# Kernel optimization log

Hardware: AMD Instinct MI355X
Metric: run time of the kernel (lower is better)

The kernel has to match this reference:

```python
import jax, jax.numpy as jnp
import numpy as np

NUM_FEAT = 64        # per-head dim == input channel C
HIDDEN = 1024        # total hidden size
NUM_HEADS = HIDDEN // NUM_FEAT  # 16


def setup_inputs() -> dict:
    key = jax.random.key(0)
    k1, k2, k3, k4, k5 = jax.random.split(key, 5)
    B, N, C = 4, 2048, NUM_FEAT
    hidden_states = jax.random.normal(k1, (B, N, C), dtype=jnp.float32)
    # nn.Linear(num_feat, hidden*3): weight [3*hidden, num_feat], store transposed for x @ W
    s_qkv = 1.0 / np.sqrt(C)
    qkv_w = jax.random.uniform(k2, (C, 3 * HIDDEN), jnp.float32, -s_qkv, s_qkv)
    qkv_b = jax.random.uniform(k3, (3 * HIDDEN,), jnp.float32, -s_qkv, s_qkv)
    s_out = 1.0 / np.sqrt(HIDDEN)
    out_w = jax.random.uniform(k4, (HIDDEN, C), jnp.float32, -s_out, s_out)
    out_b = jax.random.uniform(k5, (C,), jnp.float32, -s_out, s_out)
    return {"hidden_states": hidden_states, "qkv_w": qkv_w, "qkv_b": qkv_b,
            "out_w": out_w, "out_b": out_b}


def reference(hidden_states, qkv_w, qkv_b, out_w, out_b):
    B, N, C = hidden_states.shape
    H, D = NUM_HEADS, NUM_FEAT  # head count, head dim
    # qkv projection: [B,N,3*HIDDEN] -> [3,B,H,N,D]
    qkv = hidden_states @ qkv_w + qkv_b
    qkv = qkv.reshape(B, N, 3, H, D).transpose(2, 0, 3, 1, 4)
    q, k, v = qkv[0], qkv[1], qkv[2]
    # scaled dot-product attention with materialized scores (faithful to source)
    scores = jnp.einsum('bhqd,bhkd->bhqk', q, k) / jnp.sqrt(jnp.float32(D))
    probs = jax.nn.softmax(scores, axis=-1)
    ctx = jnp.einsum('bhqk,bhkd->bhqd', probs, v)           # [B,H,N,D]
    ctx = ctx.transpose(0, 2, 1, 3).reshape(B, N, H * D)    # [B,N,HIDDEN]
    out = ctx @ out_w + out_b                               # [B,N,C]
    return jax.nn.gelu(out, approximate=False)
```

## Files before the change

kernel.cpp:

```cpp
#include <hip/hip_runtime.h>
#include <math.h>

#define B_ 4
#define N_ 2048
#define C_ 64
#define H_ 16
#define D_ 64
#define HID 1024

#define QSCALE 0.18033688011112042f

typedef short bf16x8 __attribute__((ext_vector_type(8)));
typedef unsigned short u16x8 __attribute__((ext_vector_type(8)));
typedef float f32x4 __attribute__((ext_vector_type(4)));

#define MFMA(a, b, c) __builtin_amdgcn_mfma_f32_16x16x32_bf16((a), (b), (c), 0, 0, 0)

typedef __attribute__((address_space(3))) void lds_t;
typedef const __attribute__((address_space(1))) void gbl_t;
#define ASYNC16(g, l) __builtin_amdgcn_global_load_lds((gbl_t*)(g), (lds_t*)(l), 16, 0, 0)

static __device__ __forceinline__ unsigned short f2bf(float f) {
  unsigned u = __float_as_uint(f);
  u += 0x7FFFu + ((u >> 16) & 1u);
  return (unsigned short)(u >> 16);
}
static __device__ __forceinline__ float bf2f(unsigned short h) {
  return __uint_as_float((unsigned)h << 16);
}
static __device__ __forceinline__ unsigned pkbf(float a, float b) {
  return __builtin_amdgcn_perm(__float_as_uint(b), __float_as_uint(a),
                               0x07060302u);
}

__global__ __launch_bounds__(256, 2) void qkv_kernel(
    const float* __restrict__ X, const float* __restrict__ W,
    const float* __restrict__ bias, const float* __restrict__ W2,
    unsigned short* __restrict__ Qhi, unsigned short* __restrict__ Khi,
    unsigned short* __restrict__ Vhi,
    unsigned short* __restrict__ W2THi, unsigned short* __restrict__ W2TLo) {
  const int t = threadIdx.x;
  const int ct = blockIdx.x;
  const int tt = blockIdx.y;

  if (ct == 24) {
    int idx0 = tt * 1024 + t * 4;
#pragma unroll
    for (int e = 0; e < 4; ++e) {
      int idx = idx0 + e;
      int k = idx & 1023, col = idx >> 10;
      float v = W2[(size_t)k * 64 + col];
      unsigned short hi = f2bf(v);
      W2THi[(size_t)col * 1024 + k] = hi;
      W2TLo[(size_t)col * 1024 + k] = f2bf(v - bf2f(hi));
    }
    return;
  }

  __shared__ unsigned short qsmem[32768];
  unsigned short* sXhi = qsmem;
  unsigned short* sXlo = qsmem + 8192;
  unsigned short* sWhi = qsmem + 16384;
  unsigned short* sWlo = qsmem + 24576;

  {
    const int kg = t & 7, r0 = t >> 3;
#pragma unroll
    for (int i = 0; i < 4; ++i) {
      int row = r0 + i * 32;
      const float* src = &X[(size_t)(tt * 128 + row) * 64 + kg * 8];
      f32x4 a = *(const f32x4*)src;
      f32x4 b = *(const f32x4*)(src + 4);
      u16x8 hi8, lo8;
#pragma unroll
      for (int j = 0; j < 4; ++j) {
        hi8[j] = f2bf(a[j]);
        lo8[j] = f2bf(a[j] - bf2f(hi8[j]));
        hi8[4 + j] = f2bf(b[j]);
        lo8[4 + j] = f2bf(b[j] - bf2f(hi8[4 + j]));
      }
      int off = row * 64 + ((kg ^ (row & 7)) << 3);
      *(u16x8*)&sXhi[off] = hi8;
      *(u16x8*)&sXlo[off] = lo8;
    }
  }
  {
    const int col = t & 127, kg0 = t >> 7;
#pragma unroll
    for (int i = 0; i < 4; ++i) {
      int kg = kg0 + i * 2;
      u16x8 hi8, lo8;
#pragma unroll
      for (int j = 0; j < 8; ++j) {
        float v = W[(size_t)(kg * 8 + j) * 3072 + ct * 128 + col];
        unsigned short h = f2bf(v);
        hi8[j] = h;
        lo8[j] = f2bf(v - bf2f(h));
      }
      int off = col * 64 + ((kg ^ (col & 7)) << 3);
      *(u16x8*)&sWhi[off] = hi8;
      *(u16x8*)&sWlo[off] = lo8;
    }
  }
  __syncthreads();

  const int w = t >> 6, lane = t & 63;
  const int lid = lane & 15, quad = lane >> 4;

  bf16x8 xa[2][2][2];
#pragma unroll
  for (int mt = 0; mt < 2; ++mt) {
    int row = w * 32 + mt * 16 + lid;
#pragma unroll
    for (int kc = 0; kc < 2; ++kc) {
      int off = row * 64 + (((kc * 4 + quad) ^ (row & 7)) << 3);
      xa[mt][kc][0] = *(const bf16x8*)&sXhi[off];
      xa[mt][kc][1] = *(const bf16x8*)&sXlo[off];
    }
  }

  f32x4 acc[2][8];
#pragma unroll
  for (int mt = 0; mt < 2; ++mt)
#pragma unroll
    for (int nt = 0; nt < 8; ++nt) acc[mt][nt] = (f32x4){0.f, 0.f, 0.f, 0.f};

#pragma unroll
  for (int nt = 0; nt < 8; ++nt) {
    int col = nt * 16 + lid;
#pragma unroll
    for (int kc = 0; kc < 2; ++kc) {
      int boff = col * 64 + (((kc * 4 + quad) ^ (col & 7)) << 3);
      bf16x8 wbh = *(const bf16x8*)&sWhi[boff];
      bf16x8 wbl = *(const bf16x8*)&sWlo[boff];
#pragma unroll
      for (int mt = 0; mt < 2; ++mt) {
        f32x4 c = acc[mt][nt];
        c = MFMA(xa[mt][kc][0], wbh, c);
        c = MFMA(xa[mt][kc][0], wbl, c);
        c = MFMA(xa[mt][kc][1], wbh, c);
        acc[mt][nt] = c;
      }
    }
  }

  __syncthreads();

  const int s = ct >> 3;
  const float scale = (s == 0) ? QSCALE : 1.0f;
  float bias_r[8];
#pragma unroll
  for (int nt = 0; nt < 8; ++nt) bias_r[nt] = bias[ct * 128 + nt * 16 + lid];

  if (s < 2) {
    unsigned short(*sOut)[136] = (unsigned short(*)[136])qsmem;
#pragma unroll
    for (int mt = 0; mt < 2; ++mt)
#pragma unroll
      for (int nt = 0; nt < 8; ++nt) {
        f32x4 v = acc[mt][nt];
#pragma unroll
        for (int r = 0; r < 4; ++r)
          sOut[w * 32 + mt * 16 + quad * 4 + r][nt * 16 + lid] =
              f2bf((v[r] + bias_r[nt]) * scale);
      }
    __syncthreads();
    const int ltok = t >> 1, half = t & 1;
    const int token = tt * 128 + ltok;
    const int bb = token >> 11, n = token & 2047;
    const int head = (ct * 2 + half) & 15;
    unsigned short* A = (s == 0) ? Qhi : Khi;
    size_t dst = ((size_t)(bb * H_ + head) * N_ + n) * D_;
    const unsigned short* srcr = &sOut[ltok][half * 64];
#pragma unroll
    for (int j = 0; j < 8; ++j)
      *(uint4*)&A[dst + j * 8] = *(const uint4*)&srcr[j * 8];
  } else {
    unsigned short(*sT)[136] = (unsigned short(*)[136])qsmem;
#pragma unroll
    for (int mt = 0; mt < 2; ++mt)
#pragma unroll
      for (int nt = 0; nt < 8; ++nt) {
        f32x4 v = acc[mt][nt];
        unsigned short h0 = f2bf(v[0] + bias_r[nt]);
        unsigned short h1 = f2bf(v[1] + bias_r[nt]);
        unsigned short h2 = f2bf(v[2] + bias_r[nt]);
        unsigned short h3 = f2bf(v[3] + bias_r[nt]);
        uint2 dw;
        dw.x = (unsigned)h0 | ((unsigned)h1 << 16);
        dw.y = (unsigned)h2 | ((unsigned)h3 << 16);
        *(uint2*)&sT[nt * 16 + lid][w * 32 + mt * 16 + quad * 4] = dw;
      }
    __syncthreads();
    const int col = t >> 1, half = t & 1;
    const int hv = (ct & 7) * 2 + (col >> 6), d = col & 63;
    const int bbv = tt >> 4;
    const int n0 = (tt & 15) * 128 + half * 64;
    size_t row = (size_t)((bbv * H_ + hv) * D_ + d);
    unsigned short* dstp = Vhi + row * (size_t)N_ + n0;
    const unsigned short* srcr = &sT[col][half * 64];
#pragma unroll
    for (int j = 0; j < 8; ++j)
      *(uint4*)(dstp + j * 8) = *(const uint4*)&srcr[j * 8];
  }
}

__global__ __launch_bounds__(256, 4) void attn_kernel(
    const unsigned short* __restrict__ Qhi, const unsigned short* __restrict__ Khi,
    const unsigned short* __restrict__ VThi,
    unsigned short* __restrict__ ctxHi, unsigned short* __restrict__ ctxLo) {
  __shared__ unsigned short smem[12288];

  const int tid = threadIdx.x;
  const int w = tid >> 6, lane = tid & 63;
  const int lid = lane & 15, quad = lane >> 4;
  const int l7 = lid & 7;
  unsigned short* sK = smem;
  unsigned short* sVt = smem + 4096;
  unsigned short* sP = smem + 8192 + w * 1024;

  const int id = blockIdx.x;
  const int bh = id & 63;
  const int qt = id >> 6;
  const int b = bh >> 4, h = bh & 15;
  const size_t base = (size_t)bh * N_ * D_;
  const int row0 = qt * 128 + w * 32;

  bf16x8 qh[2][2];
#pragma unroll
  for (int mt = 0; mt < 2; ++mt) {
    int row = row0 + mt * 16 + lid;
    const unsigned short* qph = Qhi + base + (size_t)row * D_;
#pragma unroll
    for (int kc = 0; kc < 2; ++kc)
      qh[mt][kc] = *(const bf16x8*)(qph + kc * 32 + quad * 8);
  }

  f32x4 o[2][4];
  float lacc[2] = {0.f, 0.f};
#pragma unroll
  for (int mt = 0; mt < 2; ++mt)
#pragma unroll
    for (int dnt = 0; dnt < 4; ++dnt) o[mt][dnt] = (f32x4){0.f, 0.f, 0.f, 0.f};

  const int lrow = lane >> 3;
  const int lgr = (lane & 7) ^ lrow;

  auto stage = [&](int kt_, int buf_) {
    size_t gk = base + (size_t)(kt_ * 32 + w * 8 + lrow) * 64 + lgr * 8;
    ASYNC16(Khi + gk, sK + buf_ * 2048 + (w * 8) * 64);
    int pr = w * 8 + lrow;
    int vd = pr * 2 + (lgr >> 2);
    int vk0 = (lgr & 3) * 8;
    size_t gv = base + (size_t)vd * N_ + kt_ * 32 + vk0;
    ASYNC16(VThi + gv, sVt + buf_ * 2048 + (w * 8) * 64);
  };

  stage(0, 0);

  for (int kt = 0; kt < N_ / 32; ++kt) {
    const int buf = kt & 1;
    __syncthreads();
    if (kt + 1 < N_ / 32) stage(kt + 1, buf ^ 1);

    f32x4 sc[2][2];
#pragma unroll
    for (int nt = 0; nt < 2; ++nt) {
      int key = nt * 16 + lid;
#pragma unroll
      for (int kc = 0; kc < 2; ++kc) {
        int off = key * 64 + (((kc * 4 + quad) ^ l7) << 3);
        bf16x8 kh_ = *(const bf16x8*)&sK[buf * 2048 + off];
#pragma unroll
        for (int mt = 0; mt < 2; ++mt) {
          f32x4 c = (kc == 0) ? (f32x4){0.f, 0.f, 0.f, 0.f} : sc[mt][nt];
          c = MFMA(kh_, qh[mt][kc], c);
          sc[mt][nt] = c;
        }
      }
    }

    bf16x8 pa[2];
#pragma unroll
    for (int mt = 0; mt < 2; ++mt) {
      float lsum = 0.f;
#pragma unroll
      for (int nt = 0; nt < 2; ++nt) {
        float p0 = __builtin_amdgcn_exp2f(sc[mt][nt][0]);
        float p1 = __builtin_amdgcn_exp2f(sc[mt][nt][1]);
        float p2 = __builtin_amdgcn_exp2f(sc[mt][nt][2]);
        float p3 = __builtin_amdgcn_exp2f(sc[mt][nt][3]);
        lsum += (p0 + p1) + (p2 + p3);
        uint2 dw;
        dw.x = pkbf(p0, p1);
        dw.y = pkbf(p2, p3);
        int idx = (mt * 8 + (lid >> 1)) * 64 +
                  (((nt * 2 + (quad >> 1) + 4 * (lid & 1)) ^ ((lid >> 1) & 7))
                   << 3) +
                  (quad & 1) * 4;
        *(uint2*)&sP[idx] = dw;
      }
      lsum += __shfl_xor(lsum, 16);
      lsum += __shfl_xor(lsum, 32);
      lacc[mt] += lsum;
      int ridx = (mt * 8 + (lid >> 1)) * 64 +
                 (((quad + 4 * (lid & 1)) ^ ((lid >> 1) & 7)) << 3);
      pa[mt] = *(const bf16x8*)&sP[ridx];
    }

#pragma unroll
    for (int dnt = 0; dnt < 4; ++dnt) {
      int voff = buf * 2048 + (dnt * 8 + (lid >> 1)) * 64 +
                 (((quad + (lid & 1) * 4) ^ ((lid >> 1) & 7)) << 3);
      bf16x8 vh = *(const bf16x8*)&sVt[voff];
#pragma unroll
      for (int mt = 0; mt < 2; ++mt) o[mt][dnt] = MFMA(vh, pa[mt], o[mt][dnt]);
    }
  }

  __syncthreads();
  float* scr = (float*)smem + w * 1088;
  const int erow = lane >> 2, ecq = lane & 3;
#pragma unroll
  for (int mt = 0; mt < 2; ++mt) {
    float inv = 1.0f / lacc[mt];
#pragma unroll
    for (int dnt = 0; dnt < 4; ++dnt) {
      f32x4 v = o[mt][dnt] * inv;
      *(f32x4*)&scr[lid * 68 + dnt * 16 + quad * 4] = v;
    }
    int token = b * N_ + row0 + mt * 16 + erow;
    size_t doff = (size_t)token * HID + h * 64;
#pragma unroll
    for (int i = 0; i < 4; ++i) {
      f32x4 v4 = *(const f32x4*)&scr[erow * 68 + ecq * 4 + i * 16];
      unsigned short hi_[4], lo_[4];
#pragma unroll
      for (int j = 0; j < 4; ++j) {
        hi_[j] = f2bf(v4[j]);
        lo_[j] = f2bf(v4[j] - bf2f(hi_[j]));
      }
      uint2 hw, lw;
      hw.x = (unsigned)hi_[0] | ((unsigned)hi_[1] << 16);
      hw.y = (unsigned)hi_[2] | ((unsigned)hi_[3] << 16);
      lw.x = (unsigned)lo_[0] | ((unsigned)lo_[1] << 16);
      lw.y = (unsigned)lo_[2] | ((unsigned)lo_[3] << 16);
      *(uint2*)&ctxHi[doff + ecq * 4 + i * 16] = hw;
      *(uint2*)&ctxLo[doff + ecq * 4 + i * 16] = lw;
    }
  }
}

__global__ __launch_bounds__(256) void out_kernel(
    const unsigned short* __restrict__ ctxHi, const unsigned short* __restrict__ ctxLo,
    const unsigned short* __restrict__ W2THi, const unsigned short* __restrict__ W2TLo,
    const float* __restrict__ b2, float* __restrict__ out) {
  __shared__ float sO[4][4][16][16];
  const int tid = threadIdx.x;
  const int w = tid >> 6, lane = tid & 63;
  const int lid = lane & 15, quad = lane >> 4;
  const int tok0 = blockIdx.x * 16;

  f32x4 acc[4];
#pragma unroll
  for (int nt = 0; nt < 4; ++nt) acc[nt] = (f32x4){0.f, 0.f, 0.f, 0.f};

  const size_t abase = (size_t)(tok0 + lid) * HID + w * 256 + quad * 8;

  for (int kc = 0; kc < 8; ++kc) {
    bf16x8 ah = *(const bf16x8*)&ctxHi[abase + kc * 32];
    bf16x8 al = *(const bf16x8*)&ctxLo[abase + kc * 32];
#pragma unroll
    for (int nt = 0; nt < 4; ++nt) {
      size_t boff =
          (size_t)(nt * 16 + lid) * HID + w * 256 + kc * 32 + quad * 8;
      bf16x8 bh = *(const bf16x8*)&W2THi[boff];
      bf16x8 bl = *(const bf16x8*)&W2TLo[boff];
      f32x4 c = acc[nt];
      c = MFMA(ah, bh, c);
      c = MFMA(ah, bl, c);
      c = MFMA(al, bh, c);
      acc[nt] = c;
    }
  }

#pragma unroll
  for (int nt = 0; nt < 4; ++nt)
#pragma unroll
    for (int r = 0; r < 4; ++r) sO[w][nt][quad * 4 + r][lid] = acc[nt][r];
  __syncthreads();

  const int col = tid & 63;
  const int nt = col >> 4, cl = col & 15;
#pragma unroll
  for (int rr = 0; rr < 4; ++rr) {
    int row = w * 4 + rr;
    float v = sO[0][nt][row][cl] + sO[1][nt][row][cl] + sO[2][nt][row][cl] +
              sO[3][nt][row][cl] + b2[col];
    float g = 0.5f * v * (1.0f + erff(v * 0.70710678118654752f));
    out[(size_t)(tok0 + row) * 64 + col] = g;
  }
}

extern "C" void kernel_launch(void* const* d_in, const int* in_sizes, int n_in,
                              void* d_out, int out_size, void* d_ws, size_t ws_size,
                              hipStream_t stream) {
  const float* X = (const float*)d_in[0];
  const float* qkv_w = (const float*)d_in[1];
  const float* qkv_b = (const float*)d_in[2];
  const float* out_w = (const float*)d_in[3];
  const float* out_b = (const float*)d_in[4];
  float* out = (float*)d_out;

  const size_t NE = (size_t)B_ * H_ * N_ * D_;
  unsigned short* ws16 = (unsigned short*)d_ws;
  unsigned short* Qhi = ws16 + 0 * NE;
  unsigned short* Khi = ws16 + 1 * NE;
  unsigned short* VThi = ws16 + 2 * NE;
  unsigned short* ctxHi = ws16 + 3 * NE;
  unsigned short* ctxLo = ws16 + 4 * NE;
  unsigned short* W2THi = ws16 + 5 * NE;
  unsigned short* W2TLo = W2THi + 65536;

  qkv_kernel<<<dim3(25, 64), 256, 0, stream>>>(X, qkv_w, qkv_b, out_w, Qhi,
                                               Khi, VThi, W2THi, W2TLo);
  attn_kernel<<<1024, 256, 0, stream>>>(Qhi, Khi, VThi, ctxHi, ctxLo);
  out_kernel<<<512, 256, 0, stream>>>(ctxHi, ctxLo, W2THi, W2TLo, out_b, out);
}
```

Measured before the change: 204.7 us.

## Load K/V directly into registers in single-wave attention blocks, dropping LDS staging

```diff
diff --git a/kernel.cpp b/kernel.cpp
--- a/kernel.cpp
+++ b/kernel.cpp
@@ -15,10 +15,6 @@
 typedef float f32x4 __attribute__((ext_vector_type(4)));
 
 #define MFMA(a, b, c) __builtin_amdgcn_mfma_f32_16x16x32_bf16((a), (b), (c), 0, 0, 0)
-
-typedef __attribute__((address_space(3))) void lds_t;
-typedef const __attribute__((address_space(1))) void gbl_t;
-#define ASYNC16(g, l) __builtin_amdgcn_global_load_lds((gbl_t*)(g), (lds_t*)(l), 16, 0, 0)
 
 static __device__ __forceinline__ unsigned short f2bf(float f) {
   unsigned u = __float_as_uint(f);
@@ -205,84 +201,72 @@
   }
 }
 
-__global__ __launch_bounds__(256, 4) void attn_kernel(
+__global__ __launch_bounds__(64, 2) void attn_kernel(
     const unsigned short* __restrict__ Qhi, const unsigned short* __restrict__ Khi,
     const unsigned short* __restrict__ VThi,
     unsigned short* __restrict__ ctxHi, unsigned short* __restrict__ ctxLo) {
-  __shared__ unsigned short smem[12288];
-
-  const int tid = threadIdx.x;
-  const int w = tid >> 6, lane = tid & 63;
+  __shared__ float smemf[1088];
+  unsigned short* sP = (unsigned short*)smemf;
+
+  const int lane = threadIdx.x;
   const int lid = lane & 15, quad = lane >> 4;
-  const int l7 = lid & 7;
-  unsigned short* sK = smem;
-  unsigned short* sVt = smem + 4096;
-  unsigned short* sP = smem + 8192 + w * 1024;
-
   const int id = blockIdx.x;
   const int bh = id & 63;
-  const int qt = id >> 6;
+  const int qw = id >> 6;
   const int b = bh >> 4, h = bh & 15;
   const size_t base = (size_t)bh * N_ * D_;
-  const int row0 = qt * 128 + w * 32;
-
-  bf16x8 qh[2][2];
-#pragma unroll
-  for (int mt = 0; mt < 2; ++mt) {
-    int row = row0 + mt * 16 + lid;
-    const unsigned short* qph = Qhi + base + (size_t)row * D_;
+  const int row0 = qw * 64;
+
+  bf16x8 qh[4][2];
+#pragma unroll
+  for (int mt = 0; mt < 4; ++mt) {
+    const unsigned short* qph =
+        Qhi + base + (size_t)(row0 + mt * 16 + lid) * D_;
 #pragma unroll
     for (int kc = 0; kc < 2; ++kc)
       qh[mt][kc] = *(const bf16x8*)(qph + kc * 32 + quad * 8);
   }
 
-  f32x4 o[2][4];
-  float lacc[2] = {0.f, 0.f};
-#pragma unroll
-  for (int mt = 0; mt < 2; ++mt)
+  f32x4 o[4][4];
+  float lacc[4] = {0.f, 0.f, 0.f, 0.f};
+#pragma unroll
+  for (int mt = 0; mt < 4; ++mt)
 #pragma unroll
     for (int dnt = 0; dnt < 4; ++dnt) o[mt][dnt] = (f32x4){0.f, 0.f, 0.f, 0.f};
 
-  const int lrow = lane >> 3;
-  const int lgr = (lane & 7) ^ lrow;
-
-  auto stage = [&](int kt_, int buf_) {
-    size_t gk = base + (size_t)(kt_ * 32 + w * 8 + lrow) * 64 + lgr * 8;
-    ASYNC16(Khi + gk, sK + buf_ * 2048 + (w * 8) * 64);
-    int pr = w * 8 + lrow;
-    int vd = pr * 2 + (lgr >> 2);
-    int vk0 = (lgr & 3) * 8;
-    size_t gv = base + (size_t)vd * N_ + kt_ * 32 + vk0;
-    ASYNC16(VThi + gv, sVt + buf_ * 2048 + (w * 8) * 64);
+  auto loadK = [&](int kt, bf16x8 kh[2][2]) {
+#pragma unroll
+    for (int nt = 0; nt < 2; ++nt)
+#pragma unroll
+      for (int kc = 0; kc < 2; ++kc)
+        kh[nt][kc] = *(const bf16x8*)&Khi[base +
+                                         (size_t)(kt * 32 + nt * 16 + lid) * 64 +
+                                         kc * 32 + quad * 8];
   };
 
-  stage(0, 0);
-
-  for (int kt = 0; kt < N_ / 32; ++kt) {
-    const int buf = kt & 1;
-    __syncthreads();
-    if (kt + 1 < N_ / 32) stage(kt + 1, buf ^ 1);
-
-    f32x4 sc[2][2];
-#pragma unroll
-    for (int nt = 0; nt < 2; ++nt) {
-      int key = nt * 16 + lid;
-#pragma unroll
-      for (int kc = 0; kc < 2; ++kc) {
-        int off = key * 64 + (((kc * 4 + quad) ^ l7) << 3);
-        bf16x8 kh_ = *(const bf16x8*)&sK[buf * 2048 + off];
-#pragma unroll
-        for (int mt = 0; mt < 2; ++mt) {
+  auto body = [&](int kt, bf16x8 kh[2][2]) {
+    bf16x8 vh[4];
+#pragma unroll
+    for (int dnt = 0; dnt < 4; ++dnt)
+      vh[dnt] = *(const bf16x8*)&VThi[base + (size_t)(dnt * 16 + lid) * N_ +
+                                     kt * 32 + quad * 8];
+
+    f32x4 sc[4][2];
+    __builtin_amdgcn_s_setprio(1);
+#pragma unroll
+    for (int nt = 0; nt < 2; ++nt)
+#pragma unroll
+      for (int kc = 0; kc < 2; ++kc)
+#pragma unroll
+        for (int mt = 0; mt < 4; ++mt) {
           f32x4 c = (kc == 0) ? (f32x4){0.f, 0.f, 0.f, 0.f} : sc[mt][nt];
-          c = MFMA(kh_, qh[mt][kc], c);
-          sc[mt][nt] = c;
+          sc[mt][nt] = MFMA(kh[nt][kc], qh[mt][kc], c);
         }
-      }
-    }
-
-    bf16x8 pa[2];
-#pragma unroll
-    for (int mt = 0; mt < 2; ++mt) {
+    __builtin_amdgcn_s_setprio(0);
+
+    bf16x8 pa[4];
+#pragma unroll
+    for (int mt = 0; mt < 4; ++mt) {
       float lsum = 0.f;
 #pragma unroll
       for (int nt = 0; nt < 2; ++nt) {
@@ -308,21 +292,28 @@
       pa[mt] = *(const bf16x8*)&sP[ridx];
     }
 
-#pragma unroll
-    for (int dnt = 0; dnt < 4; ++dnt) {
-      int voff = buf * 2048 + (dnt * 8 + (lid >> 1)) * 64 +
-                 (((quad + (lid & 1) * 4) ^ ((lid >> 1) & 7)) << 3);
-      bf16x8 vh = *(const bf16x8*)&sVt[voff];
-#pragma unroll
-      for (int mt = 0; mt < 2; ++mt) o[mt][dnt] = MFMA(vh, pa[mt], o[mt][dnt]);
-    }
-  }
-
-  __syncthreads();
-  float* scr = (float*)smem + w * 1088;
+    __builtin_amdgcn_s_setprio(1);
+#pragma unroll
+    for (int dnt = 0; dnt < 4; ++dnt)
+#pragma unroll
+      for (int mt = 0; mt < 4; ++mt)
+        o[mt][dnt] = MFMA(vh[dnt], pa[mt], o[mt][dnt]);
+    __builtin_amdgcn_s_setprio(0);
+  };
+
+  bf16x8 khA[2][2], khB[2][2];
+  loadK(0, khA);
+  for (int kt = 0; kt < N_ / 32; kt += 2) {
+    loadK(kt + 1, khB);
+    body(kt, khA);
+    if (kt + 2 < N_ / 32) loadK(kt + 2, khA);
+    body(kt + 1, khB);
+  }
+
+  float* scr = smemf;
   const int erow = lane >> 2, ecq = lane & 3;
 #pragma unroll
-  for (int mt = 0; mt < 2; ++mt) {
+  for (int mt = 0; mt < 4; ++mt) {
     float inv = 1.0f / lacc[mt];
 #pragma unroll
     for (int dnt = 0; dnt < 4; ++dnt) {
@@ -340,13 +331,18 @@
         hi_[j] = f2bf(v4[j]);
         lo_[j] = f2bf(v4[j] - bf2f(hi_[j]));
       }
-      uint2 hw, lw;
-      hw.x = (unsigned)hi_[0] | ((unsigned)hi_[1] << 16);
-      hw.y = (unsigned)hi_[2] | ((unsigned)hi_[3] << 16);
-      lw.x = (unsigned)lo_[0] | ((unsigned)lo_[1] << 16);
-      lw.y = (unsigned)lo_[2] | ((unsigned)lo_[3] << 16);
-      *(uint2*)&ctxHi[doff + ecq * 4 + i * 16] = hw;
-      *(uint2*)&ctxLo[doff + ecq * 4 + i * 16] = lw;
+      unsigned long long hw =
+          (unsigned long long)((unsigned)hi_[2] | ((unsigned)hi_[3] << 16))
+              << 32 |
+          ((unsigned)hi_[0] | ((unsigned)hi_[1] << 16));
+      unsigned long long lw =
+          (unsigned long long)((unsigned)lo_[2] | ((unsigned)lo_[3] << 16))
+              << 32 |
+          ((unsigned)lo_[0] | ((unsigned)lo_[1] << 16));
+      __builtin_nontemporal_store(
+          hw, (unsigned long long*)&ctxHi[doff + ecq * 4 + i * 16]);
+      __builtin_nontemporal_store(
+          lw, (unsigned long long*)&ctxLo[doff + ecq * 4 + i * 16]);
     }
   }
 }
@@ -424,6 +420,6 @@
 
   qkv_kernel<<<dim3(25, 64), 256, 0, stream>>>(X, qkv_w, qkv_b, out_w, Qhi,
                                                Khi, VThi, W2THi, W2TLo);
-  attn_kernel<<<1024, 256, 0, stream>>>(Qhi, Khi, VThi, ctxHi, ctxLo);
+  attn_kernel<<<2048, 64, 0, stream>>>(Qhi, Khi, VThi, ctxHi, ctxLo);
   out_kernel<<<512, 256, 0, stream>>>(ctxHi, ctxLo, W2THi, W2TLo, out_b, out);
 }
```

Result: slower. 253.3 us (+23.7%).
